# Kernel tuning notes

Measured on AMD Instinct MI355X. Metric: run time of the kernel, lower is better.

The kernel has to match this reference:

```python
import jax, jax.numpy as jnp
import numpy as np

REF_MIC = 0
LOAD = 0.001 / np.sqrt(2.0)  # diagonal loading added to both real and imag parts


def _to_complex(x):
    # x: (N, 2, ...) real/imag stacked -> complex (N, ...)
    return x[:, 0] + 1j * x[:, 1]


def setup_inputs() -> dict:
    key = jax.random.key(0)
    k1, k2, k3 = jax.random.split(key, 3)
    N, C, T, F = 8, 16, 300, 257
    mixture = jax.random.normal(k1, (N, 2, C, T, F), dtype=jnp.float32)
    target = jax.random.normal(k2, (N, 2, C, T, F), dtype=jnp.float32)
    steering_vector = jax.random.normal(k3, (N, 2, C, F), dtype=jnp.float32)
    return {"mixture": mixture, "target": target, "steering_vector": steering_vector}


def reference(mixture, target, steering_vector):
    N, _, C, T, F = mixture.shape
    y = _to_complex(mixture)  # (N, C, T, F)
    x = _to_complex(target)   # (N, C, T, F)

    # Spatial covariance of mixture, mean over time frames (sum/T), fused einsum
    # phi[n,f] = (1/T) * sum_t y[n,:,t,f] y[n,:,t,f]^H  -> (N, F, C, C)
    phi = jnp.einsum('nctf,ndtf->nfcd', y, jnp.conj(y)) / T
    eye = jnp.eye(C, dtype=phi.dtype)
    # original adds load to BOTH real and imag diagonals (broadcast over RI dim)
    phi = phi + (LOAD + 1j * LOAD) * eye
    phi_inv = jnp.linalg.inv(phi)  # (N, F, C, C)

    # Cross covariance between mixture and reference-mic target
    A = jnp.transpose(y, (0, 3, 2, 1))            # (N, F, T, C)
    b = jnp.transpose(x[:, REF_MIC], (0, 2, 1))   # (N, F, T)
    mu_a = jnp.mean(A, axis=(0, 2), keepdims=True)  # mean over batch and time
    mu_b = jnp.mean(b, axis=(0, 2), keepdims=True)
    # mean over T of (A-mu_a)(b-mu_b)^H -> (N, F, C)
    phi_yx0 = jnp.mean((A - mu_a) * jnp.conj(b - mu_b)[..., None], axis=2)

    # MWF weights: w = phi_inv @ phi_yx0  -> (N, F, C)
    w = jnp.einsum('nfcd,nfd->nfc', phi_inv, phi_yx0)

    # Beamform: X_bf[n,t,f] = w[n,f]^H y[n,:,t,f]
    Xbf = jnp.einsum('nfc,nctf->ntf', jnp.conj(w), y)  # (N, T, F)

    # Back to real/imag stacked (N, 2, 1, T, F) matching torch output layout
    out = jnp.stack([Xbf.real, Xbf.imag], axis=1)[:, :, None]
    return out
```

## Files before the change

kernel.cpp:

```cpp
#include <hip/hip_runtime.h>

#define N_     8
#define C_     16
#define T_     300
#define F_     257
#define CC_    256
#define TF_    (T_*F_)
#define CTF_   (C_*TF_)
#define N2CTF_ (2*CTF_)

#define FT_    32
#define NFT_   9
#define TS_    5
#define RST_   35
#define SROWS_ 88
#define SCNT_  (SROWS_*RST_)

#define MREC_  272

#define LOADC  7.0710678118654755e-04f

__device__ __forceinline__ float2 cmul(float2 a, float2 b) {
  return make_float2(a.x*b.x - a.y*b.y, a.x*b.y + a.y*b.x);
}
__device__ __forceinline__ float2 cmulc(float2 a, float2 b) {
  return make_float2(a.x*b.x + a.y*b.y, a.y*b.x - a.x*b.y);
}
__device__ __forceinline__ float2 cdiv(float2 a, float2 b) {
  float inv = 1.0f / (b.x*b.x + b.y*b.y);
  return make_float2((a.x*b.x + a.y*b.y)*inv, (a.y*b.x - a.x*b.y)*inv);
}
__device__ __forceinline__ float2 cadd(float2 a, float2 b){ return make_float2(a.x+b.x, a.y+b.y); }
__device__ __forceinline__ float2 csub(float2 a, float2 b){ return make_float2(a.x-b.x, a.y-b.y); }

template<int TCH>
__global__ __launch_bounds__(512, 1) void k1_cov(const float* __restrict__ mix,
                                                 const float* __restrict__ tgt,
                                                 float2* __restrict__ phi_p,
                                                 float2* __restrict__ syx_p,
                                                 float2* __restrict__ sy_p,
                                                 float2* __restrict__ sx_p) {
  __shared__ float2 ys[2][SCNT_];
  const int tid = threadIdx.x;
  const int ft = blockIdx.x, tc = blockIdx.y, n = blockIdx.z;
  const int fbase = ft * FT_;
  const int t0 = tc * TCH;
  const int fl = tid & 31;
  const int g  = tid >> 5;
  const int c0 = (g & 3) * 4;
  const int d0 = (g >> 2) * 4;
  const bool sThread = (g < 4);
  const bool xLoader = (tid < 256);

  const float* mixN = mix + n * N2CTF_;
  const float* tgtN = tgt + n * N2CTF_;

  const int srow = tid >> 5;
  const int f_ld = min(fbase + fl, F_ - 1);
  const float* ybase = mixN + srow * TF_ + f_ld;
  const int xts = min(srow, TS_ - 1);
  const float* xbase = tgtN + f_ld;

  float2 acc[4][4];
  #pragma unroll
  for (int i = 0; i < 4; ++i)
    #pragma unroll
    for (int j = 0; j < 4; ++j) acc[i][j] = make_float2(0.f, 0.f);
  float2 syx[4], sy[4], sx = make_float2(0.f, 0.f);
  #pragma unroll
  for (int i = 0; i < 4; ++i) { syx[i] = make_float2(0.f,0.f); sy[i] = make_float2(0.f,0.f); }

  float lr[6], li[6];
  {
    #pragma unroll
    for (int k = 0; k < TS_; ++k) {
      const float* p = ybase + (t0 + k) * F_;
      lr[k] = p[0]; li[k] = p[CTF_];
    }
    if (xLoader) { const float* p = xbase + (t0 + xts) * F_; lr[5] = p[0]; li[5] = p[CTF_]; }
    #pragma unroll
    for (int k = 0; k < TS_; ++k)
      ys[0][(k * 16 + srow) * RST_ + fl] = make_float2(lr[k], li[k]);
    if (xLoader) ys[0][(80 + srow) * RST_ + fl] = make_float2(lr[5], li[5]);
  }

  constexpr int NS = TCH / TS_;
  for (int stg = 0; stg < NS; ++stg) {
    __syncthreads();
    const bool more = (stg + 1 < NS);
    if (more) {
      const int tS = t0 + (stg + 1) * TS_;
      #pragma unroll
      for (int k = 0; k < TS_; ++k) {
        const float* p = ybase + (tS + k) * F_;
        lr[k] = p[0]; li[k] = p[CTF_];
      }
      if (xLoader) { const float* p = xbase + (tS + xts) * F_; lr[5] = p[0]; li[5] = p[CTF_]; }
    }
    const float2* buf = ys[stg & 1];
    #pragma unroll
    for (int tl = 0; tl < TS_; ++tl) {
      const int rb = tl * 16;
      float2 a[4], b[4];
      #pragma unroll
      for (int i = 0; i < 4; ++i) a[i] = buf[(rb + c0 + i) * RST_ + fl];
      #pragma unroll
      for (int j = 0; j < 4; ++j) b[j] = buf[(rb + d0 + j) * RST_ + fl];
      #pragma unroll
      for (int i = 0; i < 4; ++i)
        #pragma unroll
        for (int j = 0; j < 4; ++j) {
          acc[i][j].x += a[i].x * b[j].x + a[i].y * b[j].y;
          acc[i][j].y += a[i].y * b[j].x - a[i].x * b[j].y;
        }
      if (sThread) {
        float2 xv = buf[(80 + tl) * RST_ + fl];
        #pragma unroll
        for (int i = 0; i < 4; ++i) {
          syx[i].x += a[i].x * xv.x + a[i].y * xv.y;
          syx[i].y += a[i].y * xv.x - a[i].x * xv.y;
          sy[i].x += a[i].x; sy[i].y += a[i].y;
        }
        if (g == 0) { sx.x += xv.x; sx.y += xv.y; }
      }
    }
    if (more) {
      float2* nb = ys[(stg + 1) & 1];
      #pragma unroll
      for (int k = 0; k < TS_; ++k)
        nb[(k * 16 + srow) * RST_ + fl] = make_float2(lr[k], li[k]);
      if (xLoader) nb[(80 + srow) * RST_ + fl] = make_float2(lr[5], li[5]);
    }
  }

  const int f = fbase + fl;
  if (f < F_) {
    const int tcn = tc * N_ + n;
    float2* pb = phi_p + ((size_t)tcn * F_ + f) * CC_;
    #pragma unroll
    for (int i = 0; i < 4; ++i) {
      float2* p = pb + (c0 + i) * 16 + d0;
      #pragma unroll
      for (int j = 0; j < 4; ++j) p[j] = acc[i][j];
    }
    if (sThread) {
      float2* s1 = syx_p + ((size_t)tcn * F_ + f) * C_ + c0;
      float2* s2 = sy_p  + ((size_t)tcn * F_ + f) * C_ + c0;
      #pragma unroll
      for (int i = 0; i < 4; ++i) { s1[i] = syx[i]; s2[i] = sy[i]; }
      if (g == 0) sx_p[(size_t)tcn * F_ + f] = sx;
    }
  }
}

template<int TCP>
__global__ __launch_bounds__(256) void k2a_reduce(const float2* __restrict__ phi_p,
                                                  const float2* __restrict__ syx_p,
                                                  const float2* __restrict__ sy_p,
                                                  const float2* __restrict__ sx_p,
                                                  float2* __restrict__ Mg) {
  __shared__ float2 ld_sy[TCP * N_ * C_];
  __shared__ float2 ld_syx[TCP * C_];
  __shared__ float2 ld_sx[TCP * N_];
  __shared__ float2 muB_s, sxO_s;
  const int f = blockIdx.x, n = blockIdx.y;
  const int tid = threadIdx.x;
  const int i = tid >> 4, j = tid & 15;

  float2 s = make_float2(0.f, 0.f);
  for (int tc = 0; tc < TCP; ++tc) {
    float2 v = phi_p[((size_t)(tc * N_ + n) * F_ + f) * CC_ + tid];
    s.x += v.x; s.y += v.y;
  }
  if (i == j) { s.x += (float)T_ * LOADC; s.y += (float)T_ * LOADC; }

  for (int idx = tid; idx < TCP * N_ * C_; idx += 256) {
    int tcn = idx >> 4, c = idx & 15;
    ld_sy[idx] = sy_p[((size_t)tcn * F_ + f) * C_ + c];
  }
  for (int idx = tid; idx < TCP * C_; idx += 256) {
    int tc = idx >> 4, c = idx & 15;
    ld_syx[idx] = syx_p[((size_t)(tc * N_ + n) * F_ + f) * C_ + c];
  }
  for (int idx = tid; idx < TCP * N_; idx += 256) {
    ld_sx[idx] = sx_p[(size_t)idx * F_ + f];
  }
  __syncthreads();

  float2 muA_r = make_float2(0.f,0.f), ownY = make_float2(0.f,0.f), ownYX = make_float2(0.f,0.f);
  if (tid < 16) {
    float2 allY = make_float2(0.f,0.f);
    for (int tcn = 0; tcn < TCP * N_; ++tcn) allY = cadd(allY, ld_sy[tcn * C_ + tid]);
    for (int tc = 0; tc < TCP; ++tc) {
      ownY  = cadd(ownY,  ld_sy[(tc * N_ + n) * C_ + tid]);
      ownYX = cadd(ownYX, ld_syx[tc * C_ + tid]);
    }
    const float invNT = 1.0f / ((float)N_ * (float)T_);
    muA_r = make_float2(allY.x * invNT, allY.y * invNT);
  }
  if (tid == 16) {
    float2 own = make_float2(0.f,0.f), all = make_float2(0.f,0.f);
    for (int tc = 0; tc < TCP; ++tc)
      for (int nn = 0; nn < N_; ++nn) {
        float2 v = ld_sx[tc * N_ + nn];
        all = cadd(all, v);
        if (nn == n) own = cadd(own, v);
      }
    const float invNT = 1.0f / ((float)N_ * (float)T_);
    muB_s = make_float2(all.x * invNT, all.y * invNT);
    sxO_s = own;
  }
  __syncthreads();

  float2* dst = Mg + (size_t)(n * F_ + f) * MREC_;
  dst[tid] = s;
  if (tid < 16) {
    float2 r = ownYX;
    r = csub(r, cmulc(muA_r, sxO_s));
    r = csub(r, cmulc(ownY, muB_s));
    float2 t3 = cmulc(muA_r, muB_s);
    r.x += (float)T_ * t3.x; r.y += (float)T_ * t3.y;
    dst[256 + tid] = r;
  }
}

__global__ __launch_bounds__(64) void k2b_solve(const float2* __restrict__ Mg,
                                                float* __restrict__ wre,
                                                float* __restrict__ wim) {
  __shared__ float2 M[16 * 17];
  const int f = blockIdx.x, n = blockIdx.y;
  const int tid = threadIdx.x;
  const float2* src = Mg + (size_t)(n * F_ + f) * MREC_;
  #pragma unroll
  for (int r = 0; r < 4; ++r) {
    int idx = tid + 64 * r;
    M[(idx >> 4) * 17 + (idx & 15)] = src[idx];
  }
  if (tid < 16) M[tid * 17 + 16] = src[256 + tid];
  __syncthreads();

  const int i = tid >> 2, q = tid & 3;
  for (int k = 0; k < 16; ++k) {
    float2 fac = cdiv(M[i * 17 + k], M[k * 17 + k]);
    __syncthreads();
    if (i != k) {
      #pragma unroll
      for (int jj = 0; jj < 4; ++jj) {
        int j = q * 4 + jj;
        M[i * 17 + j] = csub(M[i * 17 + j], cmul(fac, M[k * 17 + j]));
      }
      if (q == 3) M[i * 17 + 16] = csub(M[i * 17 + 16], cmul(fac, M[k * 17 + 16]));
    }
    __syncthreads();
  }
  if (q == 0) {
    float2 w = cdiv(M[i * 17 + 16], M[i * 17 + i]);
    wre[(n * C_ + i) * F_ + f] = w.x;
    wim[(n * C_ + i) * F_ + f] = w.y;
  }
}

__global__ __launch_bounds__(256) void k3_bf(const float* __restrict__ mix,
                                             const float* __restrict__ wre,
                                             const float* __restrict__ wim,
                                             float* __restrict__ out) {
  const int t = blockIdx.x, n = blockIdx.y;
  const float* mixN = mix + n * N2CTF_;
  const float* wR = wre + n * C_ * F_;
  const float* wI = wim + n * C_ * F_;
  float* outN = out + n * 2 * TF_;
  for (int f = threadIdx.x; f < F_; f += 256) {
    const float* yb = mixN + t * F_ + f;
    float xr = 0.f, xi = 0.f;
    #pragma unroll
    for (int c = 0; c < 16; ++c) {
      float wr = wR[c * F_ + f], wi = wI[c * F_ + f];
      float yr = yb[c * TF_],    yi = yb[CTF_ + c * TF_];
      xr += wr * yr + wi * yi;
      xi += wr * yi - wi * yr;
    }
    outN[t * F_ + f] = xr;
    outN[TF_ + t * F_ + f] = xi;
  }
}

template<int TCP>
static void launch_all(const float* mix, const float* tgt, float* ws, float* out,
                       hipStream_t stream) {
  constexpr int TCH = T_ / TCP;
  static_assert(TCH * TCP == T_ && TCH % TS_ == 0, "chunking");
  float2* phi_p = (float2*)ws;
  float2* syx_p = phi_p + (size_t)TCP * N_ * F_ * CC_;
  float2* sy_p  = syx_p + (size_t)TCP * N_ * F_ * C_;
  float2* sx_p  = sy_p  + (size_t)TCP * N_ * F_ * C_;
  float2* Mg    = sx_p  + (size_t)TCP * N_ * F_;
  float*  wre   = (float*)(Mg + (size_t)N_ * F_ * MREC_);
  float*  wim   = wre + N_ * C_ * F_;
  k1_cov<TCH><<<dim3(NFT_, TCP, N_), dim3(512), 0, stream>>>(mix, tgt, phi_p, syx_p, sy_p, sx_p);
  k2a_reduce<TCP><<<dim3(F_, N_), dim3(256), 0, stream>>>(phi_p, syx_p, sy_p, sx_p, Mg);
  k2b_solve<<<dim3(F_, N_), dim3(64), 0, stream>>>(Mg, wre, wim);
  k3_bf<<<dim3(T_, N_), dim3(256), 0, stream>>>(mix, wre, wim, out);
}

static size_t ws_need_bytes(int tcp) {
  size_t fl2 = (size_t)tcp * N_ * F_ * (CC_ + C_ + C_ + 1) + (size_t)N_ * F_ * MREC_;
  return fl2 * 8 + 2ull * N_ * C_ * F_ * 4;
}

extern "C" void kernel_launch(void* const* d_in, const int* in_sizes, int n_in,
                              void* d_out, int out_size, void* d_ws, size_t ws_size,
                              hipStream_t stream) {
  const float* mix = (const float*)d_in[0];
  const float* tgt = (const float*)d_in[1];
  float* out = (float*)d_out;
  float* ws  = (float*)d_ws;
  if (ws_size >= ws_need_bytes(12))      launch_all<12>(mix, tgt, ws, out, stream);
  else if (ws_size >= ws_need_bytes(6))  launch_all<6>(mix, tgt, ws, out, stream);
  else if (ws_size >= ws_need_bytes(2))  launch_all<2>(mix, tgt, ws, out, stream);
  else                                   launch_all<1>(mix, tgt, ws, out, stream);
}
```

Measured before the change: 252.0 us.

## Exploit Hermitian symmetry in covariance kernel, store lower-triangle tiles only

The covariance kernel now computes only the 10 lower-triangular 4x4 tiles of the Hermitian 16x16 matrix, using 320 threads instead of 512. Partial results are stored in a packed 160-entry layout, and the reduce kernel rebuilds the full matrix by conjugating mirrored entries. The aim is to cut FMA work and partial-sum traffic by roughly 40%. The beamform kernel also handles two time frames per block, so the weights are loaded once into registers and reused, and the time chunking changes from 12 to 10 chunks. The shared-memory load pattern is reorganised to fit the smaller thread count, which raises the number of loads per thread.

```diff
diff --git a/kernel.cpp b/kernel.cpp
--- a/kernel.cpp
+++ b/kernel.cpp
@@ -4,7 +4,6 @@
 #define C_     16
 #define T_     300
 #define F_     257
-#define CC_    256
 #define TF_    (T_*F_)
 #define CTF_   (C_*TF_)
 #define N2CTF_ (2*CTF_)
@@ -15,6 +14,8 @@
 #define RST_   35
 #define SROWS_ 88
 #define SCNT_  (SROWS_*RST_)
+#define NTILE_ 10
+#define PHIC_  (NTILE_*16)
 
 #define MREC_  272
 
@@ -34,7 +35,7 @@
 __device__ __forceinline__ float2 csub(float2 a, float2 b){ return make_float2(a.x-b.x, a.y-b.y); }
 
 template<int TCH>
-__global__ __launch_bounds__(512, 1) void k1_cov(const float* __restrict__ mix,
+__global__ __launch_bounds__(320, 1) void k1_cov(const float* __restrict__ mix,
                                                  const float* __restrict__ tgt,
                                                  float2* __restrict__ phi_p,
                                                  float2* __restrict__ syx_p,
@@ -47,18 +48,21 @@
   const int t0 = tc * TCH;
   const int fl = tid & 31;
   const int g  = tid >> 5;
-  const int c0 = (g & 3) * 4;
-  const int d0 = (g >> 2) * 4;
-  const bool sThread = (g < 4);
-  const bool xLoader = (tid < 256);
+  int ti = 0, tj = g;
+  while (tj > ti) { ++ti; tj -= ti; }
+  const int c0 = ti * 4;
+  const int d0 = tj * 4;
+  const bool sThread = (tj == 0);
+  const bool xg = (g < 5);
 
   const float* mixN = mix + n * N2CTF_;
   const float* tgtN = tgt + n * N2CTF_;
 
-  const int srow = tid >> 5;
+  const int ts_g   = g >> 1;
+  const int c_base = (g & 1) * 8;
+  const int row0   = ts_g * 16 + c_base;
   const int f_ld = min(fbase + fl, F_ - 1);
-  const float* ybase = mixN + srow * TF_ + f_ld;
-  const int xts = min(srow, TS_ - 1);
+  const float* ybase = mixN + c_base * TF_ + f_ld;
   const float* xbase = tgtN + f_ld;
 
   float2 acc[4][4];
@@ -70,18 +74,18 @@
   #pragma unroll
   for (int i = 0; i < 4; ++i) { syx[i] = make_float2(0.f,0.f); sy[i] = make_float2(0.f,0.f); }
 
-  float lr[6], li[6];
+  float lr[9], li[9];
   {
     #pragma unroll
-    for (int k = 0; k < TS_; ++k) {
-      const float* p = ybase + (t0 + k) * F_;
+    for (int k = 0; k < 8; ++k) {
+      const float* p = ybase + k * TF_ + (t0 + ts_g) * F_;
       lr[k] = p[0]; li[k] = p[CTF_];
     }
-    if (xLoader) { const float* p = xbase + (t0 + xts) * F_; lr[5] = p[0]; li[5] = p[CTF_]; }
-    #pragma unroll
-    for (int k = 0; k < TS_; ++k)
-      ys[0][(k * 16 + srow) * RST_ + fl] = make_float2(lr[k], li[k]);
-    if (xLoader) ys[0][(80 + srow) * RST_ + fl] = make_float2(lr[5], li[5]);
+    if (xg) { const float* p = xbase + (t0 + g) * F_; lr[8] = p[0]; li[8] = p[CTF_]; }
+    #pragma unroll
+    for (int k = 0; k < 8; ++k)
+      ys[0][(row0 + k) * RST_ + fl] = make_float2(lr[k], li[k]);
+    if (xg) ys[0][(80 + g) * RST_ + fl] = make_float2(lr[8], li[8]);
   }
 
   constexpr int NS = TCH / TS_;
@@ -91,11 +95,11 @@
     if (more) {
       const int tS = t0 + (stg + 1) * TS_;
       #pragma unroll
-      for (int k = 0; k < TS_; ++k) {
-        const float* p = ybase + (tS + k) * F_;
+      for (int k = 0; k < 8; ++k) {
+        const float* p = ybase + k * TF_ + (tS + ts_g) * F_;
         lr[k] = p[0]; li[k] = p[CTF_];
       }
-      if (xLoader) { const float* p = xbase + (tS + xts) * F_; lr[5] = p[0]; li[5] = p[CTF_]; }
+      if (xg) { const float* p = xbase + (tS + g) * F_; lr[8] = p[0]; li[8] = p[CTF_]; }
     }
     const float2* buf = ys[stg & 1];
     #pragma unroll
@@ -127,22 +131,20 @@
     if (more) {
       float2* nb = ys[(stg + 1) & 1];
       #pragma unroll
-      for (int k = 0; k < TS_; ++k)
-        nb[(k * 16 + srow) * RST_ + fl] = make_float2(lr[k], li[k]);
-      if (xLoader) nb[(80 + srow) * RST_ + fl] = make_float2(lr[5], li[5]);
+      for (int k = 0; k < 8; ++k)
+        nb[(row0 + k) * RST_ + fl] = make_float2(lr[k], li[k]);
+      if (xg) nb[(80 + g) * RST_ + fl] = make_float2(lr[8], li[8]);
     }
   }
 
   const int f = fbase + fl;
   if (f < F_) {
     const int tcn = tc * N_ + n;
-    float2* pb = phi_p + ((size_t)tcn * F_ + f) * CC_;
-    #pragma unroll
-    for (int i = 0; i < 4; ++i) {
-      float2* p = pb + (c0 + i) * 16 + d0;
-      #pragma unroll
-      for (int j = 0; j < 4; ++j) p[j] = acc[i][j];
-    }
+    float2* pb = phi_p + ((size_t)tcn * F_ + f) * PHIC_ + g * 16;
+    #pragma unroll
+    for (int i = 0; i < 4; ++i)
+      #pragma unroll
+      for (int j = 0; j < 4; ++j) pb[i * 4 + j] = acc[i][j];
     if (sThread) {
       float2* s1 = syx_p + ((size_t)tcn * F_ + f) * C_ + c0;
       float2* s2 = sy_p  + ((size_t)tcn * F_ + f) * C_ + c0;
@@ -167,11 +169,18 @@
   const int tid = threadIdx.x;
   const int i = tid >> 4, j = tid & 15;
 
+  const int ti = i >> 2, tj = j >> 2, ci = i & 3, cj = j & 3;
+  int gL, cell; bool cj_flip;
+  if (ti >= tj) { gL = ti * (ti + 1) / 2 + tj; cell = ci * 4 + cj; cj_flip = false; }
+  else          { gL = tj * (tj + 1) / 2 + ti; cell = cj * 4 + ci; cj_flip = true; }
+  const int off = gL * 16 + cell;
+
   float2 s = make_float2(0.f, 0.f);
   for (int tc = 0; tc < TCP; ++tc) {
-    float2 v = phi_p[((size_t)(tc * N_ + n) * F_ + f) * CC_ + tid];
+    float2 v = phi_p[((size_t)(tc * N_ + n) * F_ + f) * PHIC_ + off];
     s.x += v.x; s.y += v.y;
   }
+  if (cj_flip) s.y = -s.y;
   if (i == j) { s.x += (float)T_ * LOADC; s.y += (float)T_ * LOADC; }
 
   for (int idx = tid; idx < TCP * N_ * C_; idx += 256) {
@@ -264,23 +273,30 @@
                                              const float* __restrict__ wre,
                                              const float* __restrict__ wim,
                                              float* __restrict__ out) {
-  const int t = blockIdx.x, n = blockIdx.y;
+  const int t0 = blockIdx.x * 2, n = blockIdx.y;
   const float* mixN = mix + n * N2CTF_;
   const float* wR = wre + n * C_ * F_;
   const float* wI = wim + n * C_ * F_;
   float* outN = out + n * 2 * TF_;
   for (int f = threadIdx.x; f < F_; f += 256) {
-    const float* yb = mixN + t * F_ + f;
-    float xr = 0.f, xi = 0.f;
+    float wr[16], wi[16];
+    #pragma unroll
+    for (int c = 0; c < 16; ++c) { wr[c] = wR[c * F_ + f]; wi[c] = wI[c * F_ + f]; }
+    const float* yb = mixN + t0 * F_ + f;
+    float xr0 = 0.f, xi0 = 0.f, xr1 = 0.f, xi1 = 0.f;
     #pragma unroll
     for (int c = 0; c < 16; ++c) {
-      float wr = wR[c * F_ + f], wi = wI[c * F_ + f];
-      float yr = yb[c * TF_],    yi = yb[CTF_ + c * TF_];
-      xr += wr * yr + wi * yi;
-      xi += wr * yi - wi * yr;
-    }
-    outN[t * F_ + f] = xr;
-    outN[TF_ + t * F_ + f] = xi;
+      float yr0 = yb[c * TF_],      yi0 = yb[CTF_ + c * TF_];
+      float yr1 = yb[c * TF_ + F_], yi1 = yb[CTF_ + c * TF_ + F_];
+      xr0 += wr[c] * yr0 + wi[c] * yi0;
+      xi0 += wr[c] * yi0 - wi[c] * yr0;
+      xr1 += wr[c] * yr1 + wi[c] * yi1;
+      xi1 += wr[c] * yi1 - wi[c] * yr1;
+    }
+    outN[t0 * F_ + f] = xr0;
+    outN[TF_ + t0 * F_ + f] = xi0;
+    outN[(t0 + 1) * F_ + f] = xr1;
+    outN[TF_ + (t0 + 1) * F_ + f] = xi1;
   }
 }
 
@@ -290,20 +306,20 @@
   constexpr int TCH = T_ / TCP;
   static_assert(TCH * TCP == T_ && TCH % TS_ == 0, "chunking");
   float2* phi_p = (float2*)ws;
-  float2* syx_p = phi_p + (size_t)TCP * N_ * F_ * CC_;
+  float2* syx_p = phi_p + (size_t)TCP * N_ * F_ * PHIC_;
   float2* sy_p  = syx_p + (size_t)TCP * N_ * F_ * C_;
   float2* sx_p  = sy_p  + (size_t)TCP * N_ * F_ * C_;
   float2* Mg    = sx_p  + (size_t)TCP * N_ * F_;
   float*  wre   = (float*)(Mg + (size_t)N_ * F_ * MREC_);
   float*  wim   = wre + N_ * C_ * F_;
-  k1_cov<TCH><<<dim3(NFT_, TCP, N_), dim3(512), 0, stream>>>(mix, tgt, phi_p, syx_p, sy_p, sx_p);
+  k1_cov<TCH><<<dim3(NFT_, TCP, N_), dim3(320), 0, stream>>>(mix, tgt, phi_p, syx_p, sy_p, sx_p);
   k2a_reduce<TCP><<<dim3(F_, N_), dim3(256), 0, stream>>>(phi_p, syx_p, sy_p, sx_p, Mg);
   k2b_solve<<<dim3(F_, N_), dim3(64), 0, stream>>>(Mg, wre, wim);
-  k3_bf<<<dim3(T_, N_), dim3(256), 0, stream>>>(mix, wre, wim, out);
+  k3_bf<<<dim3(T_ / 2, N_), dim3(256), 0, stream>>>(mix, wre, wim, out);
 }
 
 static size_t ws_need_bytes(int tcp) {
-  size_t fl2 = (size_t)tcp * N_ * F_ * (CC_ + C_ + C_ + 1) + (size_t)N_ * F_ * MREC_;
+  size_t fl2 = (size_t)tcp * N_ * F_ * (PHIC_ + C_ + C_ + 1) + (size_t)N_ * F_ * MREC_;
   return fl2 * 8 + 2ull * N_ * C_ * F_ * 4;
 }
 
@@ -314,8 +330,8 @@
   const float* tgt = (const float*)d_in[1];
   float* out = (float*)d_out;
   float* ws  = (float*)d_ws;
-  if (ws_size >= ws_need_bytes(12))      launch_all<12>(mix, tgt, ws, out, stream);
-  else if (ws_size >= ws_need_bytes(6))  launch_all<6>(mix, tgt, ws, out, stream);
+  if (ws_size >= ws_need_bytes(10))      launch_all<10>(mix, tgt, ws, out, stream);
+  else if (ws_size >= ws_need_bytes(5))  launch_all<5>(mix, tgt, ws, out, stream);
   else if (ws_size >= ws_need_bytes(2))  launch_all<2>(mix, tgt, ws, out, stream);
   else                                   launch_all<1>(mix, tgt, ws, out, stream);
 }
```

After: 240.0 us. -4.7%, faster.
